# Kernel tuning notes

Hardware: AMD Instinct MI355X
Metric: run time of the kernel (lower is better)

## Reference

```python
import jax, jax.numpy as jnp
import numpy as np

N = 100000; E = 1600000; IN = 64; H = 128; G = 64

def setup_inputs() -> dict:
    key = jax.random.key(0)
    ks = jax.random.split(key, 8)
    h = jax.random.normal(ks[0], (N, IN), jnp.float32)
    src = jax.random.randint(ks[1], (E,), 0, N, jnp.int32)
    dst = jax.random.randint(ks[2], (E,), 0, N, jnp.int32)
    graph_ids = jnp.sort(jax.random.randint(ks[3], (N,), 0, G, jnp.int32))
    W1 = jax.random.normal(ks[4], (IN, H), jnp.float32) / jnp.sqrt(IN)
    b1 = jnp.zeros((H,), jnp.float32)
    W2 = jax.random.normal(ks[5], (H, H), jnp.float32) / jnp.sqrt(H)
    b2 = jnp.zeros((H,), jnp.float32)
    Wr = jax.random.normal(ks[6], (H, 1), jnp.float32) / jnp.sqrt(H)
    br = jnp.zeros((1,), jnp.float32)
    return {"h": h, "src": src, "dst": dst, "graph_ids": graph_ids, "num_graphs": G,
            "W1": W1, "b1": b1, "W2": W2, "b2": b2, "Wr": Wr, "br": br}

def _gcn(x, src, dst, inv_sqrt_out, inv_sqrt_in, W, b):
    # DGL GraphConv, norm='both', aggregate-first (in_feats <= out_feats):
    # out = D_in^{-1/2} * A * (D_out^{-1/2} * x) @ W + b
    x = x * inv_sqrt_out[:, None]
    agg = jax.ops.segment_sum(x[src], dst, num_segments=x.shape[0])  # [N, d]
    return agg @ W * inv_sqrt_in[:, None] + b

def reference(h, src, dst, graph_ids, num_graphs, W1, b1, W2, b2, Wr, br):
    n = h.shape[0]
    ones_e = jnp.ones(src.shape[0], h.dtype)
    deg_out = jnp.maximum(jax.ops.segment_sum(ones_e, src, num_segments=n), 1.0)
    deg_in = jnp.maximum(jax.ops.segment_sum(ones_e, dst, num_segments=n), 1.0)
    iso = jax.lax.rsqrt(deg_out)
    isi = jax.lax.rsqrt(deg_in)
    h1 = jax.nn.relu(_gcn(h, src, dst, iso, isi, W1, b1))   # conv1 has activation=relu
    h2 = _gcn(h1, src, dst, iso, isi, W2, b2)               # conv2 has no activation
    hf = jax.nn.relu(h2)                                    # outer F.relu in forward
    # mean_nodes: per-graph mean readout
    sums = jax.ops.segment_sum(hf, graph_ids, num_segments=num_graphs)  # [G, H]
    cnt = jnp.maximum(jax.ops.segment_sum(jnp.ones(n, hf.dtype), graph_ids, num_segments=num_graphs), 1.0)
    hg = sums / cnt[:, None]
    return hg @ Wr + br  # [G, 1]
```

## Files before the change

### kernel.cpp

```cpp
#include <hip/hip_runtime.h>

#define N_IN 64
#define N_H  128
#define N_G  64
#define HP   4
#define HC   64
#define YSTRIDE 132

#define SWZB(r) (((r) & 7) << 3)

typedef unsigned int   uint32;
typedef unsigned short ushort16;
typedef unsigned char  uchar8;
typedef float floatx2 __attribute__((ext_vector_type(2)));
typedef short bf16x8 __attribute__((ext_vector_type(8)));
typedef float f32x4  __attribute__((ext_vector_type(4)));

#define FP8_SCALE    32.0f
#define FP8_INVSCALE 0.03125f

#if defined(__has_builtin)
#if __has_builtin(__builtin_amdgcn_cvt_pk_f32_fp8) && __has_builtin(__builtin_amdgcn_cvt_pk_fp8_f32)
#define HW_FP8 1
#endif
#endif

__device__ __forceinline__ float bf2f(ushort16 u) {
    union { uint32 i; float f; } x; x.i = ((uint32)u) << 16; return x.f;
}
__device__ __forceinline__ ushort16 f2bf(float f) {
    union { float f; uint32 i; } x; x.f = f;
    uint32 r = x.i + 0x7FFFu + ((x.i >> 16) & 1u);
    return (ushort16)(r >> 16);
}

#ifndef HW_FP8
__device__ __forceinline__ uint32 f2e4m3(float x) {
    union { float f; uint32 i; } v; v.f = x;
    uint32 s = (v.i >> 24) & 0x80u;
    uint32 a = v.i & 0x7FFFFFFFu;
    if (a < 0x3C000000u) return s;
    uint32 r = a + 0x0007FFFFu + ((a >> 20) & 1u);
    int e = (int)(r >> 23) - 120;
    if (e <= 0) return s;
    if (e > 15) return s | 0x7Eu;
    return s | ((uint32)e << 3) | ((r >> 20) & 7u);
}
__device__ __forceinline__ floatx2 e4m3word(uint32 u, bool hi) {
    floatx2 o;
    uint32 w = hi ? (u >> 16) : u;
    #pragma unroll
    for (int k = 0; k < 2; ++k) {
        uint32 b = (w >> (8 * k)) & 0xFFu;
        uint32 m = b & 0x7Fu;
        union { uint32 i; float f; } x;
        x.i = ((b & 0x80u) << 24) | ((m << 20) + 0x3C000000u);
        o[k] = m ? x.f : 0.f;
    }
    return o;
}
#endif

__device__ __forceinline__ uint32 pack4fp8(float o0, float o1, float o2, float o3) {
#ifdef HW_FP8
    int r = __builtin_amdgcn_cvt_pk_fp8_f32(o0, o1, 0, false);
    r     = __builtin_amdgcn_cvt_pk_fp8_f32(o2, o3, r, true);
    return (uint32)r;
#else
    return f2e4m3(o0) | (f2e4m3(o1) << 8) | (f2e4m3(o2) << 16) | (f2e4m3(o3) << 24);
#endif
}


__global__ __launch_bounds__(1024) void hist_kernel(const int* __restrict__ src,
        const int* __restrict__ dst, ushort16* __restrict__ part_cnt,
        int N, int E, int npp, int ec) {
    extern __shared__ int cnt[];
    int p = blockIdx.x & (HP - 1);
    int c = blockIdx.x >> 2;
    int nlo = p * npp;
    int nhi = min(nlo + npp, N);
    int nn = nhi - nlo;
    if (nn <= 0) return;
    int tid = threadIdx.x;
    for (int i = tid; i < nn; i += 1024) cnt[i] = 0;
    __syncthreads();
    int elo = c * ec, ehi = min(elo + ec, E);
    for (int e = elo + tid; e < ehi; e += 1024) {
        int s = src[e];
        unsigned so = (unsigned)(s - nlo);
        if (so < (unsigned)nn) atomicAdd(&cnt[so], 1);
        int d = dst[e];
        unsigned dof = (unsigned)(d - nlo);
        if (dof < (unsigned)nn) atomicAdd(&cnt[dof], 1 << 16);
    }
    __syncthreads();
    for (int i = tid; i < nn; i += 1024) {
        int v = cnt[i];
        part_cnt[(size_t)c * N + nlo + i] =
            (ushort16)((v & 0xFF) | ((v >> 8) & 0xFF00));
    }
}

__global__ void reduce_norm_kernel(const ushort16* __restrict__ part_cnt,
        uchar8* __restrict__ pre, const int* __restrict__ gid,
        float* __restrict__ iso, float* __restrict__ isi, int* __restrict__ deg_in,
        int* __restrict__ gstart, int* __restrict__ gend, int N) {
    int n = blockIdx.x * blockDim.x + threadIdx.x;
    if (n >= N) return;
    int so = 0, si = 0;
    #pragma unroll
    for (int c = 0; c < HC; ++c) {
        int v = part_cnt[(size_t)c * N + n];
        so += v & 0xFF;
        pre[(size_t)c * N + n] = (uchar8)si;
        si += v >> 8;
    }
    iso[n] = rsqrtf((float)max(so, 1));
    isi[n] = rsqrtf((float)max(si, 1));
    deg_in[n] = si;
    int g = gid[n];
    if (n == 0 || gid[n - 1] != g) gstart[g] = n;
    if (n == N - 1 || gid[n + 1] != g) gend[g] = n + 1;
}

__global__ __launch_bounds__(1024) void scan_partial(const int* __restrict__ deg_in,
                                                     int* __restrict__ bsum, int N) {
    int i = blockIdx.x * 1024 + threadIdx.x;
    int v = (i < N) ? deg_in[i] : 0;
    int lane = threadIdx.x & 63, wv = threadIdx.x >> 6;
    int s = v;
    #pragma unroll
    for (int off = 1; off < 64; off <<= 1) s += __shfl_xor(s, off);
    __shared__ int ws[16];
    if (lane == 0) ws[wv] = s;
    __syncthreads();
    if (threadIdx.x == 0) {
        int t = 0;
        #pragma unroll
        for (int k = 0; k < 16; ++k) t += ws[k];
        bsum[blockIdx.x] = t;
    }
}

__global__ void scan_bsum(int* __restrict__ bsum, int nb) {
    int tid = threadIdx.x;
    int lane = tid & 63, wv = tid >> 6;
    int v = (tid < nb) ? bsum[tid] : 0;
    int s = v;
    #pragma unroll
    for (int off = 1; off < 64; off <<= 1) {
        int t = __shfl_up(s, off);
        if (lane >= off) s += t;
    }
    __shared__ int w0tot;
    if (wv == 0 && lane == 63) w0tot = s;
    __syncthreads();
    if (wv == 1) s += w0tot;
    if (tid < nb) bsum[tid] = s - v;
}

__global__ __launch_bounds__(1024) void scan_write(const int* __restrict__ deg_in,
                                                   const int* __restrict__ bsum,
                                                   int* __restrict__ row_ptr, int N) {
    int i = blockIdx.x * 1024 + threadIdx.x;
    int v = (i < N) ? deg_in[i] : 0;
    int lane = threadIdx.x & 63, wv = threadIdx.x >> 6;
    int s = v;
    #pragma unroll
    for (int off = 1; off < 64; off <<= 1) {
        int t = __shfl_up(s, off);
        if (lane >= off) s += t;
    }
    __shared__ int ws[16];
    if (lane == 63) ws[wv] = s;
    __syncthreads();
    if (wv == 0 && lane < 16) {
        int x = ws[lane];
        int s2 = x;
        #pragma unroll
        for (int off = 1; off < 16; off <<= 1) {
            int t = __shfl_up(s2, off);
            if (lane >= off) s2 += t;
        }
        ws[lane] = s2;
    }
    __syncthreads();
    int base = bsum[blockIdx.x] + (wv > 0 ? ws[wv - 1] : 0);
    if (i < N) row_ptr[i] = base + s - v;
    if (i == N - 1) row_ptr[N] = base + s;
}

__global__ __launch_bounds__(1024) void fill_kernel(const int* __restrict__ src,
        const int* __restrict__ dst, const int* __restrict__ row_ptr,
        const uchar8* __restrict__ pre, int* __restrict__ col,
        int N, int E, int npp, int ec) {
    extern __shared__ int cur[];
    int p = blockIdx.x & (HP - 1);
    int c = blockIdx.x >> 2;
    int nlo = p * npp;
    int nhi = min(nlo + npp, N);
    int nn = nhi - nlo;
    if (nn <= 0) return;
    int tid = threadIdx.x;
    for (int i = tid; i < nn; i += 1024)
        cur[i] = row_ptr[nlo + i] + (int)pre[(size_t)c * N + nlo + i];
    __syncthreads();
    int elo = c * ec, ehi = min(elo + ec, E);
    for (int e = elo + tid; e < ehi; e += 1024) {
        int d = dst[e];
        unsigned off = (unsigned)(d - nlo);
        if (off < (unsigned)nn) {
            int slot = atomicAdd(&cur[off], 1);
            col[slot] = src[e];
        }
    }
}

__global__ __launch_bounds__(256) void scale_h_kernel(const float* __restrict__ h,
        const float* __restrict__ iso, ushort16* __restrict__ hs, int N) {
    int t = blockIdx.x * 256 + threadIdx.x;
    int base = t * 8;
    if (base >= N * N_IN) return;
    int n = base >> 6;
    float s = iso[n];
    float4 a = *(const float4*)&h[base];
    float4 b = *(const float4*)&h[base + 4];
    uint4 pk;
    pk.x = (uint32)f2bf(a.x * s) | ((uint32)f2bf(a.y * s) << 16);
    pk.y = (uint32)f2bf(a.z * s) | ((uint32)f2bf(a.w * s) << 16);
    pk.z = (uint32)f2bf(b.x * s) | ((uint32)f2bf(b.y * s) << 16);
    pk.w = (uint32)f2bf(b.z * s) | ((uint32)f2bf(b.w * s) << 16);
    *(uint4*)&hs[base] = pk;
}

__global__ __launch_bounds__(1024) void wprep_kernel(const float* __restrict__ W1,
        const float* __restrict__ W2, ushort16* __restrict__ W1T,
        ushort16* __restrict__ W2T) {
    int t = blockIdx.x * 1024 + threadIdx.x;
    if (t < 128 * 128) {
        int j = t >> 7, k = t & 127;
        W2T[j * 128 + k] = f2bf(W2[k * 128 + j]);
    } else if (t < 128 * 128 + 128 * 64) {
        int q = t - 128 * 128;
        int j = q >> 6, k = q & 63;
        W1T[j * 64 + k] = f2bf(W1[k * 128 + j]);
    }
}


__global__ __launch_bounds__(256) void gather1_kernel(const uint32* __restrict__ hsw,
        const int* __restrict__ row_ptr, const int* __restrict__ col,
        uint32* __restrict__ agg1w, int N) {
    int wave = __builtin_amdgcn_readfirstlane(threadIdx.x >> 6);
    int lane = threadIdx.x & 63;
    int half = lane >> 5, l32 = lane & 31;
    int n = blockIdx.x * 4 + wave;
    if (n >= N) return;
    int p0 = row_ptr[n], p1 = row_ptr[n + 1];
    float a0 = 0.f, a1 = 0.f;
    for (int pb = p0; pb < p1; pb += 64) {
        int cnt = min(64, p1 - pb);
        int cv = col[min(pb + lane, p1 - 1)];
        for (int i0 = 0; i0 < cnt; i0 += 16) {
            int   sidx[8];
            float w[8];
            #pragma unroll
            for (int i = 0; i < 8; ++i) {
                int q = i0 + 2 * i + half;
                sidx[i] = __shfl(cv, min(q, cnt - 1));
                w[i] = (q < cnt) ? 1.f : 0.f;
            }
            uint32 u[8];
            #pragma unroll
            for (int i = 0; i < 8; ++i)
                u[i] = hsw[(size_t)sidx[i] * 32 + l32];
            #pragma unroll
            for (int i = 0; i < 8; ++i) {
                union { uint32 i; float f; } lo, hi;
                lo.i = u[i] << 16;
                hi.i = u[i] & 0xFFFF0000u;
                a0 = fmaf(lo.f, w[i], a0);
                a1 = fmaf(hi.f, w[i], a1);
            }
        }
    }
    a0 += __shfl_xor(a0, 32);
    a1 += __shfl_xor(a1, 32);
    if (half == 0)
        agg1w[(size_t)n * 32 + l32] = (uint32)f2bf(a0) | ((uint32)f2bf(a1) << 16);
}

__global__ __launch_bounds__(256) void gather2_kernel(const uint32* __restrict__ h18w,
        const int* __restrict__ row_ptr, const int* __restrict__ col,
        uint32* __restrict__ agg2w, int N) {
    int wave = __builtin_amdgcn_readfirstlane(threadIdx.x >> 6);
    int lane = threadIdx.x & 63;
    int half = lane >> 5, l32 = lane & 31;
    int n = blockIdx.x * 4 + wave;
    if (n >= N) return;
    int p0 = row_ptr[n], p1 = row_ptr[n + 1];
    float a0 = 0.f, a1 = 0.f, a2 = 0.f, a3 = 0.f;
    for (int pb = p0; pb < p1; pb += 64) {
        int cnt = min(64, p1 - pb);
        int cv = col[min(pb + lane, p1 - 1)];
        for (int i0 = 0; i0 < cnt; i0 += 16) {
            int   sidx[8];
            float w[8];
            #pragma unroll
            for (int i = 0; i < 8; ++i) {
                int q = i0 + 2 * i + half;
                sidx[i] = __shfl(cv, min(q, cnt - 1));
                w[i] = (q < cnt) ? FP8_INVSCALE : 0.f;
            }
            uint32 u[8];
            #pragma unroll
            for (int i = 0; i < 8; ++i)
                u[i] = h18w[(size_t)sidx[i] * 32 + l32];
            #pragma unroll
            for (int i = 0; i < 8; ++i) {
#ifdef HW_FP8
                floatx2 dlo = __builtin_amdgcn_cvt_pk_f32_fp8((int)u[i], false);
                floatx2 dhi = __builtin_amdgcn_cvt_pk_f32_fp8((int)u[i], true);
#else
                floatx2 dlo = e4m3word(u[i], false);
                floatx2 dhi = e4m3word(u[i], true);
#endif
                a0 = fmaf(dlo.x, w[i], a0);
                a1 = fmaf(dlo.y, w[i], a1);
                a2 = fmaf(dhi.x, w[i], a2);
                a3 = fmaf(dhi.y, w[i], a3);
            }
        }
    }
    a0 += __shfl_xor(a0, 32);
    a1 += __shfl_xor(a1, 32);
    a2 += __shfl_xor(a2, 32);
    a3 += __shfl_xor(a3, 32);
    if (half == 0) {
        uint32 w0 = (uint32)f2bf(a0) | ((uint32)f2bf(a1) << 16);
        uint32 w1 = (uint32)f2bf(a2) | ((uint32)f2bf(a3) << 16);
        *(uint2*)&agg2w[(size_t)n * 64 + l32 * 2] = uint2{w0, w1};
    }
}

__global__ __launch_bounds__(512) void mm1_kernel(const ushort16* __restrict__ agg1bf,
        const ushort16* __restrict__ W1T, const float* __restrict__ b1,
        const float* __restrict__ isi, const float* __restrict__ iso,
        uchar8* __restrict__ h18, int N) {
    __shared__ union {
        struct { ushort16 A[128 * 64]; ushort16 W[128 * 64]; } st;
        float Y[128 * YSTRIDE];
    } u;
    __shared__ float ISI[128], ISO[128];
    int t = threadIdx.x;
    int n0 = blockIdx.x * 128;
    {
        int r = t >> 2;
        int k0 = (t & 3) * 16;
        bool valid = (n0 + r) < N;
        const uint4* ga = (const uint4*)(agg1bf + (size_t)(n0 + r) * 64 + k0);
        const uint4* gw = (const uint4*)(W1T + (size_t)r * 64 + k0);
        #pragma unroll
        for (int q = 0; q < 2; ++q) {
            uint4 va = valid ? ga[q] : uint4{0, 0, 0, 0};
            uint4 vw = gw[q];
            int kg = k0 + q * 8;
            *(uint4*)&u.st.A[r * 64 + (kg ^ SWZB(r))] = va;
            *(uint4*)&u.st.W[r * 64 + (kg ^ SWZB(r))] = vw;
        }
        if (t < 128) {
            ISI[t] = (n0 + t < N) ? isi[n0 + t] : 0.f;
            ISO[t] = (n0 + t < N) ? iso[n0 + t] * FP8_SCALE : 0.f;
        }
    }
    __syncthreads();
    int w = __builtin_amdgcn_readfirstlane(t >> 6);
    int l = t & 63, l15 = l & 15, lhi = l >> 4;
    int jcol = w * 16 + l15;
    float b1j = b1[jcol];
    f32x4 acc[8] = {};
    #pragma unroll
    for (int kk = 0; kk < 2; ++kk) {
        int kb = kk * 32 + lhi * 8;
        bf16x8 bf = *(bf16x8*)&u.st.W[jcol * 64 + (kb ^ SWZB(jcol))];
        #pragma unroll
        for (int tm = 0; tm < 8; ++tm) {
            int row = tm * 16 + l15;
            bf16x8 af = *(bf16x8*)&u.st.A[row * 64 + (kb ^ SWZB(row))];
            acc[tm] = __builtin_amdgcn_mfma_f32_16x16x32_bf16(af, bf, acc[tm], 0, 0, 0);
        }
    }
    __syncthreads();
    #pragma unroll
    for (int tm = 0; tm < 8; ++tm) {
        #pragma unroll
        for (int i = 0; i < 4; ++i) {
            int m = tm * 16 + lhi * 4 + i;
            u.Y[m * YSTRIDE + jcol] =
                fmaxf(fmaf(acc[tm][i], ISI[m], b1j), 0.f) * ISO[m];
        }
    }
    __syncthreads();
    {
        int r = t >> 2;
        int c0 = (t & 3) * 32;
        if (n0 + r < N) {
            uint32 b[8];
            #pragma unroll
            for (int q = 0; q < 8; ++q) {
                float4 y4 = *(float4*)&u.Y[r * YSTRIDE + c0 + q * 4];
                b[q] = pack4fp8(y4.x, y4.y, y4.z, y4.w);
            }
            uchar8* dstp = h18 + (size_t)(n0 + r) * 128 + c0;
            *(uint4*)dstp        = uint4{b[0], b[1], b[2], b[3]};
            *(uint4*)(dstp + 16) = uint4{b[4], b[5], b[6], b[7]};
        }
    }
}

__global__ __launch_bounds__(512) void mm2_kernel(const uint32* __restrict__ agg2bf,
        const ushort16* __restrict__ W2T, const float* __restrict__ b2,
        const float* __restrict__ isi, const int* __restrict__ gid,
        float* __restrict__ sums, int N) {
    __shared__ union {
        struct { ushort16 A[128 * 128]; ushort16 W[128 * 128]; } st;
        float Y[128 * YSTRIDE];
    } u;
    __shared__ float ISI[128];
    int t = threadIdx.x;
    int n0 = blockIdx.x * 128;
    {
        int r = t >> 2;
        int k0 = (t & 3) * 32;
        bool valid = (n0 + r) < N;
        const uint4* ga = (const uint4*)((const ushort16*)agg2bf + (size_t)(n0 + r) * 128 + k0);
        const uint4* gw = (const uint4*)(W2T + (size_t)r * 128 + k0);
        #pragma unroll
        for (int q = 0; q < 4; ++q) {
            uint4 va = valid ? ga[q] : uint4{0, 0, 0, 0};
            uint4 vw = gw[q];
            int kg = k0 + q * 8;
            *(uint4*)&u.st.A[r * 128 + (kg ^ SWZB(r))] = va;
            *(uint4*)&u.st.W[r * 128 + (kg ^ SWZB(r))] = vw;
        }
        if (t < 128) ISI[t] = (n0 + t < N) ? isi[n0 + t] : 0.f;
    }
    __syncthreads();
    int w = __builtin_amdgcn_readfirstlane(t >> 6);
    int l = t & 63, l15 = l & 15, lhi = l >> 4;
    int jcol = w * 16 + l15;
    float b2j = b2[jcol];
    f32x4 acc[8] = {};
    #pragma unroll
    for (int kk = 0; kk < 4; ++kk) {
        int kb = kk * 32 + lhi * 8;
        bf16x8 bf = *(bf16x8*)&u.st.W[jcol * 128 + (kb ^ SWZB(jcol))];
        #pragma unroll
        for (int tm = 0; tm < 8; ++tm) {
            int row = tm * 16 + l15;
            bf16x8 af = *(bf16x8*)&u.st.A[row * 128 + (kb ^ SWZB(row))];
            acc[tm] = __builtin_amdgcn_mfma_f32_16x16x32_bf16(af, bf, acc[tm], 0, 0, 0);
        }
    }
    __syncthreads();
    #pragma unroll
    for (int tm = 0; tm < 8; ++tm) {
        #pragma unroll
        for (int i = 0; i < 4; ++i) {
            int m = tm * 16 + lhi * 4 + i;
            u.Y[m * YSTRIDE + jcol] = fmaxf(fmaf(acc[tm][i], ISI[m], b2j), 0.f);
        }
    }
    __syncthreads();
    int j = t & 127;
    int seg = t >> 7;
    float racc = 0.f;
    int cur = -1;
    for (int i = 0; i < 32; ++i) {
        int ln = seg * 32 + i;
        int n = n0 + ln;
        if (n >= N) break;
        float y = u.Y[ln * YSTRIDE + j];
        int g = gid[n];
        if (g != cur) {
            if (cur >= 0) atomicAdd(&sums[cur * N_H + j], racc);
            racc = 0.f;
            cur = g;
        }
        racc += y;
    }
    if (cur >= 0) atomicAdd(&sums[cur * N_H + j], racc);
}

__global__ void out_kernel(const float* __restrict__ sums, const int* __restrict__ gstart,
                           const int* __restrict__ gend, const float* __restrict__ Wr,
                           const float* __restrict__ br, float* __restrict__ out) {
    int g = blockIdx.x;
    int j = threadIdx.x;
    float c = fmaxf((float)(gend[g] - gstart[g]), 1.f);
    float v = sums[g * N_H + j] / c * Wr[j];
    for (int off = 32; off > 0; off >>= 1) v += __shfl_down(v, off);
    __shared__ float part[2];
    if ((threadIdx.x & 63) == 0) part[threadIdx.x >> 6] = v;
    __syncthreads();
    if (threadIdx.x == 0) out[g] = part[0] + part[1] + br[0];
}

static inline size_t align_up(size_t x, size_t a) { return (x + a - 1) & ~(a - 1); }

extern "C" void kernel_launch(void* const* d_in, const int* in_sizes, int n_in,
                              void* d_out, int out_size, void* d_ws, size_t ws_size,
                              hipStream_t stream) {
    const float* h  = (const float*)d_in[0];
    const int* src  = (const int*)d_in[1];
    const int* dst  = (const int*)d_in[2];
    const int* gid  = (const int*)d_in[3];
    const float* W1 = (const float*)d_in[5];
    const float* b1 = (const float*)d_in[6];
    const float* W2 = (const float*)d_in[7];
    const float* b2 = (const float*)d_in[8];
    const float* Wr = (const float*)d_in[9];
    const float* br = (const float*)d_in[10];
    float* out = (float*)d_out;

    int N = in_sizes[0] / N_IN;
    int E = in_sizes[1];
    int nb  = (N + 1023) / 1024;
    int npp = (N + HP - 1) / HP;
    int ec  = (E + HC - 1) / HC;
    size_t hist_lds = (size_t)npp * 4;

    char* ws = (char*)d_ws;
    size_t off = 0;
    auto alloc = [&](size_t bytes) -> char* {
        char* p = ws + off;
        off = align_up(off + bytes, 256);
        return p;
    };
    int*   gstart  = (int*)alloc((size_t)N_G * 4);
    int*   gend    = (int*)alloc((size_t)N_G * 4);
    float* sums    = (float*)alloc((size_t)N_G * N_H * 4);
    size_t zero_bytes = off;
    int*      deg_in  = (int*)alloc((size_t)N * 4);
    float*    iso     = (float*)alloc((size_t)N * 4);
    float*    isi     = (float*)alloc((size_t)N * 4);
    int*      row_ptr = (int*)alloc((size_t)(N + 1) * 4);
    int*      bsum    = (int*)alloc((size_t)128 * 4);
    int*      col     = (int*)alloc((size_t)E * 4);
    ushort16* hs      = (ushort16*)alloc((size_t)N * N_IN * 2);
    uchar8*   h18     = (uchar8*)alloc((size_t)N * N_H);
    ushort16* W1T     = (ushort16*)alloc((size_t)128 * 64 * 2);
    ushort16* W2T     = (ushort16*)alloc((size_t)128 * 128 * 2);
    ushort16* agg1bf  = (ushort16*)alloc((size_t)N * N_IN * 2);
    uint32*   agg2bf  = (uint32*)alloc((size_t)N * 64 * 4);
    ushort16* part_cnt = (ushort16*)agg1bf;
    uchar8*   pre      = (uchar8*)agg2bf;

    hipMemsetAsync(d_ws, 0, zero_bytes, stream);

    wprep_kernel<<<24, 1024, 0, stream>>>(W1, W2, W1T, W2T);
    hist_kernel<<<HP * HC, 1024, hist_lds, stream>>>(src, dst, part_cnt, N, E, npp, ec);
    reduce_norm_kernel<<<(N + 255) / 256, 256, 0, stream>>>(part_cnt, pre, gid, iso, isi,
                                                            deg_in, gstart, gend, N);
    scan_partial<<<nb, 1024, 0, stream>>>(deg_in, bsum, N);
    scan_bsum<<<1, 128, 0, stream>>>(bsum, nb);
    scan_write<<<nb, 1024, 0, stream>>>(deg_in, bsum, row_ptr, N);
    fill_kernel<<<HP * HC, 1024, hist_lds, stream>>>(src, dst, row_ptr, pre, col, N, E, npp, ec);
    scale_h_kernel<<<(N * N_IN / 8 + 255) / 256, 256, 0, stream>>>(h, iso, hs, N);

    gather1_kernel<<<(N + 3) / 4, 256, 0, stream>>>((const uint32*)hs, row_ptr, col,
                                                    (uint32*)agg1bf, N);
    mm1_kernel<<<(N + 127) / 128, 512, 0, stream>>>(agg1bf, W1T, b1, isi, iso, h18, N);
    gather2_kernel<<<(N + 3) / 4, 256, 0, stream>>>((const uint32*)h18, row_ptr, col,
                                                    agg2bf, N);
    mm2_kernel<<<(N + 127) / 128, 512, 0, stream>>>(agg2bf, W2T, b2, isi, gid, sums, N);
    out_kernel<<<N_G, N_H, 0, stream>>>(sums, gstart, gend, Wr, br, out);
}
```

Baseline: 202.1 us.

## Store scaled layer-1 features as FP8 and streamline gather inner loops

The scaled input features are now stored as scaled E4M3 FP8 instead of bf16, which halves the bytes gathered per edge in the first aggregation. Gather1 is reorganized so 16 lanes cover one 64-byte row, letting each wave fetch four neighbours per step. Both gathers now precompute byte offsets and split out a full-block loop that skips the per-edge weight multiply, with the FP8 inverse scale applied once at the end. The cost is extra quantization error on the first-layer inputs.

Measured after the change: 190.3 us. 1.06x faster.

```diff
diff --git a/kernel.cpp b/kernel.cpp
--- a/kernel.cpp
+++ b/kernel.cpp
@@ -60,6 +60,21 @@
     return o;
 }
 #endif
+
+__device__ __forceinline__ floatx2 fp8lo(uint32 u) {
+#ifdef HW_FP8
+    return __builtin_amdgcn_cvt_pk_f32_fp8((int)u, false);
+#else
+    return e4m3word(u, false);
+#endif
+}
+__device__ __forceinline__ floatx2 fp8hi(uint32 u) {
+#ifdef HW_FP8
+    return __builtin_amdgcn_cvt_pk_f32_fp8((int)u, true);
+#else
+    return e4m3word(u, true);
+#endif
+}
 
 __device__ __forceinline__ uint32 pack4fp8(float o0, float o1, float o2, float o3) {
 #ifdef HW_FP8
@@ -218,20 +233,18 @@
 }
 
 __global__ __launch_bounds__(256) void scale_h_kernel(const float* __restrict__ h,
-        const float* __restrict__ iso, ushort16* __restrict__ hs, int N) {
+        const float* __restrict__ iso, uchar8* __restrict__ hs8, int N) {
     int t = blockIdx.x * 256 + threadIdx.x;
     int base = t * 8;
     if (base >= N * N_IN) return;
     int n = base >> 6;
-    float s = iso[n];
+    float s = iso[n] * FP8_SCALE;
     float4 a = *(const float4*)&h[base];
     float4 b = *(const float4*)&h[base + 4];
-    uint4 pk;
-    pk.x = (uint32)f2bf(a.x * s) | ((uint32)f2bf(a.y * s) << 16);
-    pk.y = (uint32)f2bf(a.z * s) | ((uint32)f2bf(a.w * s) << 16);
-    pk.z = (uint32)f2bf(b.x * s) | ((uint32)f2bf(b.y * s) << 16);
-    pk.w = (uint32)f2bf(b.z * s) | ((uint32)f2bf(b.w * s) << 16);
-    *(uint4*)&hs[base] = pk;
+    uint2 pk;
+    pk.x = pack4fp8(a.x * s, a.y * s, a.z * s, a.w * s);
+    pk.y = pack4fp8(b.x * s, b.y * s, b.z * s, b.w * s);
+    *(uint2*)&hs8[base] = pk;
 }
 
 __global__ __launch_bounds__(1024) void wprep_kernel(const float* __restrict__ W1,
@@ -248,50 +261,70 @@
     }
 }
 
-
-__global__ __launch_bounds__(256) void gather1_kernel(const uint32* __restrict__ hsw,
+__global__ __launch_bounds__(256) void gather1_kernel(const uchar8* __restrict__ hs8,
         const int* __restrict__ row_ptr, const int* __restrict__ col,
         uint32* __restrict__ agg1w, int N) {
     int wave = __builtin_amdgcn_readfirstlane(threadIdx.x >> 6);
     int lane = threadIdx.x & 63;
-    int half = lane >> 5, l32 = lane & 31;
+    int qd = lane >> 4, l16 = lane & 15;
     int n = blockIdx.x * 4 + wave;
     if (n >= N) return;
     int p0 = row_ptr[n], p1 = row_ptr[n + 1];
-    float a0 = 0.f, a1 = 0.f;
+    uint32 lofs = (uint32)l16 * 4;
+    float a0 = 0.f, a1 = 0.f, a2 = 0.f, a3 = 0.f;
     for (int pb = p0; pb < p1; pb += 64) {
         int cnt = min(64, p1 - pb);
-        int cv = col[min(pb + lane, p1 - 1)];
-        for (int i0 = 0; i0 < cnt; i0 += 16) {
-            int   sidx[8];
-            float w[8];
-            #pragma unroll
-            for (int i = 0; i < 8; ++i) {
-                int q = i0 + 2 * i + half;
-                sidx[i] = __shfl(cv, min(q, cnt - 1));
+        uint32 cvoff = ((uint32)col[min(pb + lane, p1 - 1)]) << 6;
+        int i0 = 0;
+        for (; i0 + 16 <= cnt; i0 += 16) {
+            uint32 off[4], u[4];
+            #pragma unroll
+            for (int i = 0; i < 4; ++i)
+                off[i] = __shfl(cvoff, i0 + 4 * i + qd);
+            #pragma unroll
+            for (int i = 0; i < 4; ++i)
+                u[i] = *(const uint32*)((const char*)hs8 + (off[i] + lofs));
+            #pragma unroll
+            for (int i = 0; i < 4; ++i) {
+                floatx2 dlo = fp8lo(u[i]), dhi = fp8hi(u[i]);
+                a0 += dlo.x; a1 += dlo.y; a2 += dhi.x; a3 += dhi.y;
+            }
+        }
+        if (i0 < cnt) {
+            uint32 off[4], u[4];
+            float w[4];
+            #pragma unroll
+            for (int i = 0; i < 4; ++i) {
+                int q = i0 + 4 * i + qd;
+                off[i] = __shfl(cvoff, min(q, cnt - 1));
                 w[i] = (q < cnt) ? 1.f : 0.f;
             }
-            uint32 u[8];
-            #pragma unroll
-            for (int i = 0; i < 8; ++i)
-                u[i] = hsw[(size_t)sidx[i] * 32 + l32];
-            #pragma unroll
-            for (int i = 0; i < 8; ++i) {
-                union { uint32 i; float f; } lo, hi;
-                lo.i = u[i] << 16;
-                hi.i = u[i] & 0xFFFF0000u;
-                a0 = fmaf(lo.f, w[i], a0);
-                a1 = fmaf(hi.f, w[i], a1);
+            #pragma unroll
+            for (int i = 0; i < 4; ++i)
+                u[i] = *(const uint32*)((const char*)hs8 + (off[i] + lofs));
+            #pragma unroll
+            for (int i = 0; i < 4; ++i) {
+                floatx2 dlo = fp8lo(u[i]), dhi = fp8hi(u[i]);
+                a0 = fmaf(dlo.x, w[i], a0);
+                a1 = fmaf(dlo.y, w[i], a1);
+                a2 = fmaf(dhi.x, w[i], a2);
+                a3 = fmaf(dhi.y, w[i], a3);
             }
         }
     }
-    a0 += __shfl_xor(a0, 32);
-    a1 += __shfl_xor(a1, 32);
-    if (half == 0)
-        agg1w[(size_t)n * 32 + l32] = (uint32)f2bf(a0) | ((uint32)f2bf(a1) << 16);
-}
-
-__global__ __launch_bounds__(256) void gather2_kernel(const uint32* __restrict__ h18w,
+    a0 += __shfl_xor(a0, 16); a0 += __shfl_xor(a0, 32);
+    a1 += __shfl_xor(a1, 16); a1 += __shfl_xor(a1, 32);
+    a2 += __shfl_xor(a2, 16); a2 += __shfl_xor(a2, 32);
+    a3 += __shfl_xor(a3, 16); a3 += __shfl_xor(a3, 32);
+    if (lane < 16) {
+        a0 *= FP8_INVSCALE; a1 *= FP8_INVSCALE; a2 *= FP8_INVSCALE; a3 *= FP8_INVSCALE;
+        uint32 w0 = (uint32)f2bf(a0) | ((uint32)f2bf(a1) << 16);
+        uint32 w1 = (uint32)f2bf(a2) | ((uint32)f2bf(a3) << 16);
+        *(uint2*)&agg1w[(size_t)n * 32 + l16 * 2] = uint2{w0, w1};
+    }
+}
+
+__global__ __launch_bounds__(256) void gather2_kernel(const uchar8* __restrict__ h18,
         const int* __restrict__ row_ptr, const int* __restrict__ col,
         uint32* __restrict__ agg2w, int N) {
     int wave = __builtin_amdgcn_readfirstlane(threadIdx.x >> 6);
@@ -300,32 +333,41 @@
     int n = blockIdx.x * 4 + wave;
     if (n >= N) return;
     int p0 = row_ptr[n], p1 = row_ptr[n + 1];
+    uint32 lofs = (uint32)l32 * 4;
     float a0 = 0.f, a1 = 0.f, a2 = 0.f, a3 = 0.f;
     for (int pb = p0; pb < p1; pb += 64) {
         int cnt = min(64, p1 - pb);
-        int cv = col[min(pb + lane, p1 - 1)];
-        for (int i0 = 0; i0 < cnt; i0 += 16) {
-            int   sidx[8];
+        uint32 cvoff = ((uint32)col[min(pb + lane, p1 - 1)]) << 7;
+        int i0 = 0;
+        for (; i0 + 16 <= cnt; i0 += 16) {
+            uint32 off[8], u[8];
+            #pragma unroll
+            for (int i = 0; i < 8; ++i)
+                off[i] = __shfl(cvoff, i0 + 2 * i + half);
+            #pragma unroll
+            for (int i = 0; i < 8; ++i)
+                u[i] = *(const uint32*)((const char*)h18 + (off[i] + lofs));
+            #pragma unroll
+            for (int i = 0; i < 8; ++i) {
+                floatx2 dlo = fp8lo(u[i]), dhi = fp8hi(u[i]);
+                a0 += dlo.x; a1 += dlo.y; a2 += dhi.x; a3 += dhi.y;
+            }
+        }
+        if (i0 < cnt) {
+            uint32 off[8], u[8];
             float w[8];
             #pragma unroll
             for (int i = 0; i < 8; ++i) {
                 int q = i0 + 2 * i + half;
-                sidx[i] = __shfl(cv, min(q, cnt - 1));
-                w[i] = (q < cnt) ? FP8_INVSCALE : 0.f;
+                off[i] = __shfl(cvoff, min(q, cnt - 1));
+                w[i] = (q < cnt) ? 1.f : 0.f;
             }
-            uint32 u[8];
             #pragma unroll
             for (int i = 0; i < 8; ++i)
-                u[i] = h18w[(size_t)sidx[i] * 32 + l32];
+                u[i] = *(const uint32*)((const char*)h18 + (off[i] + lofs));
             #pragma unroll
             for (int i = 0; i < 8; ++i) {
-#ifdef HW_FP8
-                floatx2 dlo = __builtin_amdgcn_cvt_pk_f32_fp8((int)u[i], false);
-                floatx2 dhi = __builtin_amdgcn_cvt_pk_f32_fp8((int)u[i], true);
-#else
-                floatx2 dlo = e4m3word(u[i], false);
-                floatx2 dhi = e4m3word(u[i], true);
-#endif
+                floatx2 dlo = fp8lo(u[i]), dhi = fp8hi(u[i]);
                 a0 = fmaf(dlo.x, w[i], a0);
                 a1 = fmaf(dlo.y, w[i], a1);
                 a2 = fmaf(dhi.x, w[i], a2);
@@ -338,6 +380,7 @@
     a2 += __shfl_xor(a2, 32);
     a3 += __shfl_xor(a3, 32);
     if (half == 0) {
+        a0 *= FP8_INVSCALE; a1 *= FP8_INVSCALE; a2 *= FP8_INVSCALE; a3 *= FP8_INVSCALE;
         uint32 w0 = (uint32)f2bf(a0) | ((uint32)f2bf(a1) << 16);
         uint32 w1 = (uint32)f2bf(a2) | ((uint32)f2bf(a3) << 16);
         *(uint2*)&agg2w[(size_t)n * 64 + l32 * 2] = uint2{w0, w1};
@@ -548,7 +591,7 @@
     int*      row_ptr = (int*)alloc((size_t)(N + 1) * 4);
     int*      bsum    = (int*)alloc((size_t)128 * 4);
     int*      col     = (int*)alloc((size_t)E * 4);
-    ushort16* hs      = (ushort16*)alloc((size_t)N * N_IN * 2);
+    uchar8*   hs8     = (uchar8*)alloc((size_t)N * N_IN);
     uchar8*   h18     = (uchar8*)alloc((size_t)N * N_H);
     ushort16* W1T     = (ushort16*)alloc((size_t)128 * 64 * 2);
     ushort16* W2T     = (ushort16*)alloc((size_t)128 * 128 * 2);
@@ -567,13 +610,11 @@
     scan_bsum<<<1, 128, 0, stream>>>(bsum, nb);
     scan_write<<<nb, 1024, 0, stream>>>(deg_in, bsum, row_ptr, N);
     fill_kernel<<<HP * HC, 1024, hist_lds, stream>>>(src, dst, row_ptr, pre, col, N, E, npp, ec);
-    scale_h_kernel<<<(N * N_IN / 8 + 255) / 256, 256, 0, stream>>>(h, iso, hs, N);
-
-    gather1_kernel<<<(N + 3) / 4, 256, 0, stream>>>((const uint32*)hs, row_ptr, col,
-                                                    (uint32*)agg1bf, N);
+    scale_h_kernel<<<(N * N_IN / 8 + 255) / 256, 256, 0, stream>>>(h, iso, hs8, N);
+
+    gather1_kernel<<<(N + 3) / 4, 256, 0, stream>>>(hs8, row_ptr, col, (uint32*)agg1bf, N);
     mm1_kernel<<<(N + 127) / 128, 512, 0, stream>>>(agg1bf, W1T, b1, isi, iso, h18, N);
-    gather2_kernel<<<(N + 3) / 4, 256, 0, stream>>>((const uint32*)h18, row_ptr, col,
-                                                    agg2bf, N);
+    gather2_kernel<<<(N + 3) / 4, 256, 0, stream>>>(h18, row_ptr, col, agg2bf, N);
     mm2_kernel<<<(N + 127) / 128, 512, 0, stream>>>(agg2bf, W2T, b2, isi, gid, sums, N);
     out_kernel<<<N_G, N_H, 0, stream>>>(sums, gstart, gend, Wr, br, out);
 }
```
